# Optimization experiments

Hardware: AMD Instinct MI355X
Metric: run time of the kernel (lower is better)

The kernel has to match this reference:

```python
import jax, jax.numpy as jnp
import numpy as np

# Norse-style LIF constants (LIFParameters defaults, method='super', alpha=100)
DT = 0.001
TAU_SYN_INV = 200.0
TAU_MEM_INV = 100.0
V_TH = 1.0
V_LEAK = 0.0
V_RESET = 0.0
ALPHA = 100.0

@jax.custom_vjp
def heaviside(x):
    return (x > 0).astype(x.dtype)

def _heaviside_fwd(x):
    return heaviside(x), x

def _heaviside_bwd(x, g):
    # SuperSpike surrogate: 1 / (alpha*|x| + 1)^2
    return (g / (ALPHA * jnp.abs(x) + 1.0) ** 2,)

heaviside.defvjp(_heaviside_fwd, _heaviside_bwd)

def lif_step(v, i, inp_cur):
    # explicit-Euler LIF: membrane decays toward leak driven by synaptic current,
    # synaptic current decays, spikes reset membrane, input arrives as current jump
    v_dec = v + DT * TAU_MEM_INV * ((V_LEAK - v) + i)
    i_dec = i * (1.0 - DT * TAU_SYN_INV)
    z = heaviside(v_dec - V_TH)
    v_new = (1.0 - z) * v_dec + z * V_RESET
    i_new = i_dec + inp_cur
    return z, v_new, i_new

def li_step(v, i, inp_cur):
    # leaky integrator (non-spiking readout)
    v_new = v + DT * TAU_MEM_INV * ((V_LEAK - v) + i)
    i_new = i * (1.0 - DT * TAU_SYN_INV) + inp_cur
    return v_new, i_new


def setup_inputs() -> dict:
    key = jax.random.key(0)
    k1, k2, k3 = jax.random.split(key, 3)
    T, B = 64, 128
    FS2, H1, HC, OC, OUT = 4096, 2048, 2, 4, 10
    spl1, spl2 = FS2 // HC, H1 // OC
    x = jax.random.uniform(k1, (T, B, FS2), dtype=jnp.float32)
    w_hidden = jax.random.normal(k2, (HC, spl1, H1), dtype=jnp.float32) / np.sqrt(spl1)
    w_out = jax.random.normal(k3, (OC, spl2, OUT), dtype=jnp.float32) / np.sqrt(spl2)
    return {"x": x, "w_hidden": w_hidden, "w_out": w_out}


def reference(x, w_hidden, w_out):
    T, B, FS2 = x.shape
    HC, SPL1, H1 = w_hidden.shape
    OC, SPL2, OUT = w_out.shape
    f32 = x.dtype

    def step(carry, x_t):
        vdh, idh, vsh, ish, vdo, ido, vso, iso = carry
        # split input across hidden dendritic channels: [HC, B, SPL1]
        zc = x_t.reshape(B, HC, SPL1).transpose(1, 0, 2)
        cur_h = jnp.einsum('cbi,cio->cbo', zc, w_hidden)      # [HC, B, H1]
        s_d, vdh, idh = lif_step(vdh, idh, cur_h)             # dendritic spikes
        z_s, vsh, ish = lif_step(vsh, ish, s_d.sum(0))        # somatic spikes [B, H1]
        # split hidden spikes across output dendritic channels: [OC, B, SPL2]
        zo = z_s.reshape(B, OC, SPL2).transpose(1, 0, 2)
        cur_o = jnp.einsum('cbi,cio->cbo', zo, w_out)         # [OC, B, OUT]
        s_o, vdo, ido = lif_step(vdo, ido, cur_o)
        vso, iso = li_step(vso, iso, s_o.sum(0))              # readout voltage [B, OUT]
        return (vdh, idh, vsh, ish, vdo, ido, vso, iso), vso

    z = jnp.zeros
    carry0 = (z((HC, B, H1), f32), z((HC, B, H1), f32),
              z((B, H1), f32), z((B, H1), f32),
              z((OC, B, OUT), f32), z((OC, B, OUT), f32),
              z((B, OUT), f32), z((B, OUT), f32))
    _, voltages = jax.lax.scan(step, carry0, x)
    return voltages  # [T, B, 10]
```

## Files before the change

kernel.cpp:

```cpp
#include <hip/hip_runtime.h>

#define B 128
#define HC 2
#define H1 2048
#define FS2 4096
#define NK 2048
#define OC 4
#define SPL2 512
#define NOUT 10
#define T 64
#define HBH (HC*B*H1)

typedef __attribute__((ext_vector_type(8))) short bf16x8;
typedef __attribute__((ext_vector_type(4))) float f32x4;

__device__ __forceinline__ unsigned short f2bf(float f) {
  unsigned u = __float_as_uint(f);
  u += 0x7fff + ((u >> 16) & 1);
  return (unsigned short)(u >> 16);
}
__device__ __forceinline__ float bf2f(unsigned short s) {
  return __uint_as_float(((unsigned)s) << 16);
}

__device__ __forceinline__ void gload16(const void* g, void* l) {
  __builtin_amdgcn_global_load_lds(
      (const __attribute__((address_space(1))) unsigned int*)g,
      (__attribute__((address_space(3))) unsigned int*)l, 16, 0, 0);
}

__global__ __launch_bounds__(256) void init_state(float* __restrict__ p, int n) {
  int i = blockIdx.x * 256 + threadIdx.x;
  if (i < n) p[i] = 0.f;
}

__global__ __launch_bounds__(256) void conv_x(
    const float4* __restrict__ xin, ushort4* __restrict__ xh,
    ushort4* __restrict__ xl, int n4) {
  for (int i = blockIdx.x * 256 + threadIdx.x; i < n4; i += gridDim.x * 256) {
    float4 v = xin[i];
    ushort4 h, lo;
    h.x = f2bf(v.x); h.y = f2bf(v.y); h.z = f2bf(v.z); h.w = f2bf(v.w);
    lo.x = f2bf(v.x - bf2f(h.x)); lo.y = f2bf(v.y - bf2f(h.y));
    lo.z = f2bf(v.z - bf2f(h.z)); lo.w = f2bf(v.w - bf2f(h.w));
    xh[i] = h; xl[i] = lo;
  }
}

__global__ __launch_bounds__(256) void conv_w(
    const float* __restrict__ w, unsigned short* __restrict__ wth,
    unsigned short* __restrict__ wtl) {
  __shared__ float s[64][65];
  const int c = blockIdx.z;
  const int n0 = blockIdx.x * 64, k0 = blockIdx.y * 64;
  const int tid = threadIdx.x;
  const int r = tid >> 4, c4 = (tid & 15) * 4;
#pragma unroll
  for (int q = 0; q < 4; ++q) {
    int kr = r + q * 16;
    float4 v = *(const float4*)(w + ((size_t)c * NK + k0 + kr) * H1 + n0 + c4);
    s[kr][c4 + 0] = v.x; s[kr][c4 + 1] = v.y;
    s[kr][c4 + 2] = v.z; s[kr][c4 + 3] = v.w;
  }
  __syncthreads();
#pragma unroll
  for (int q = 0; q < 4; ++q) {
    int nr = r + q * 16;
    float a0 = s[c4 + 0][nr], a1 = s[c4 + 1][nr];
    float a2 = s[c4 + 2][nr], a3 = s[c4 + 3][nr];
    ushort4 h, lo;
    h.x = f2bf(a0); h.y = f2bf(a1); h.z = f2bf(a2); h.w = f2bf(a3);
    lo.x = f2bf(a0 - bf2f(h.x)); lo.y = f2bf(a1 - bf2f(h.y));
    lo.z = f2bf(a2 - bf2f(h.z)); lo.w = f2bf(a3 - bf2f(h.w));
    size_t off = ((size_t)c * H1 + n0 + nr) * NK + k0 + c4;
    *(ushort4*)(wth + off) = h;
    *(ushort4*)(wtl + off) = lo;
  }
}

__global__ __launch_bounds__(512, 2) void gemm_split(
    const unsigned short* __restrict__ xh, const unsigned short* __restrict__ xl,
    const unsigned short* __restrict__ wth, const unsigned short* __restrict__ wtl,
    float* __restrict__ cur, int Mc, int nMblk) {
  const int bid = blockIdx.x;
  int c, nb, mb;
  if ((nMblk & 3) == 0) {
    const int xcd = bid & 7;
    const int slot = bid >> 3;
    c = xcd & 1;
    const int q = xcd >> 1;
    const int mq = nMblk >> 2;
    nb = slot & 7;
    mb = q * mq + (slot >> 3);
  } else {
    mb = bid % nMblk;
    int rest = bid / nMblk;
    nb = rest & 7;
    c = rest >> 3;
  }
  const int bm = mb * 256, bn = nb * 256;

  __shared__ unsigned short lds[65536];
  const int tid = threadIdx.x;

  unsigned dstOff[2]; size_t srcA[2], srcB[2];
#pragma unroll
  for (int q = 0; q < 2; ++q) {
    int idx = q * 512 + tid;
    int row = idx >> 2, ps = idx & 3;
    int ks = (ps - (row >> 1)) & 3;
    int ar = bm + row; if (ar > Mc - 1) ar = Mc - 1;
    srcA[q] = (size_t)ar * FS2 + (size_t)c * NK + ks * 8;
    srcB[q] = (size_t)c * NK * H1 + (size_t)(bn + row) * NK + ks * 8;
    dstOff[q] = idx * 8;
  }

  const int l = tid & 63, w = tid >> 6;
  const int wr = w >> 2, wc = w & 3;
  const int lrow = l & 15, lks = l >> 4;
  unsigned aoff[8], boff[4];
#pragma unroll
  for (int m = 0; m < 8; ++m) {
    int row = wr * 128 + m * 16 + lrow;
    int ps = (lks + (row >> 1)) & 3;
    aoff[m] = row * 32 + ps * 8;
  }
#pragma unroll
  for (int n = 0; n < 4; ++n) {
    int rn = wc * 64 + n * 16 + lrow;
    int ps = (lks + (rn >> 1)) & 3;
    boff[n] = rn * 32 + ps * 8;
  }

  f32x4 acc[8][4];
#pragma unroll
  for (int m = 0; m < 8; ++m)
#pragma unroll
    for (int n = 0; n < 4; ++n) acc[m][n] = (f32x4){0.f, 0.f, 0.f, 0.f};

#pragma unroll
  for (int q = 0; q < 2; ++q) {
    gload16(xh + srcA[q], &lds[dstOff[q]]);
    gload16(xl + srcA[q], &lds[8192 + dstOff[q]]);
    gload16(wth + srcB[q], &lds[16384 + dstOff[q]]);
    gload16(wtl + srcB[q], &lds[24576 + dstOff[q]]);
  }
  __syncthreads();

  const int NT = NK / 32;
  int curb = 0;
  for (int kt = 0; kt < NT; ++kt) {
    if (kt + 1 < NT) {
      const int k0 = (kt + 1) * 32;
      const unsigned nb0 = (curb ^ 1) * 32768;
#pragma unroll
      for (int q = 0; q < 2; ++q) {
        gload16(xh + srcA[q] + k0, &lds[nb0 + dstOff[q]]);
        gload16(xl + srcA[q] + k0, &lds[nb0 + 8192 + dstOff[q]]);
        gload16(wth + srcB[q] + k0, &lds[nb0 + 16384 + dstOff[q]]);
        gload16(wtl + srcB[q] + k0, &lds[nb0 + 24576 + dstOff[q]]);
      }
    }
    const unsigned short* bc = &lds[curb * 32768];
    bf16x8 bh[4], bl[4];
#pragma unroll
    for (int n = 0; n < 4; ++n) {
      bh[n] = *(const bf16x8*)&bc[16384 + boff[n]];
      bl[n] = *(const bf16x8*)&bc[24576 + boff[n]];
    }
#pragma unroll
    for (int mh = 0; mh < 2; ++mh) {
      bf16x8 ah[4], al[4];
#pragma unroll
      for (int mm = 0; mm < 4; ++mm) {
        ah[mm] = *(const bf16x8*)&bc[aoff[mh * 4 + mm]];
        al[mm] = *(const bf16x8*)&bc[8192 + aoff[mh * 4 + mm]];
      }
#pragma unroll
      for (int mm = 0; mm < 4; ++mm)
#pragma unroll
        for (int n = 0; n < 4; ++n) {
          int m = mh * 4 + mm;
          acc[m][n] = __builtin_amdgcn_mfma_f32_16x16x32_bf16(ah[mm], bh[n], acc[m][n], 0, 0, 0);
          acc[m][n] = __builtin_amdgcn_mfma_f32_16x16x32_bf16(ah[mm], bl[n], acc[m][n], 0, 0, 0);
          acc[m][n] = __builtin_amdgcn_mfma_f32_16x16x32_bf16(al[mm], bh[n], acc[m][n], 0, 0, 0);
        }
    }
    __syncthreads();
    curb ^= 1;
  }

  float* Cc = cur + (size_t)c * Mc * H1;
#pragma unroll
  for (int m = 0; m < 8; ++m) {
    int grow = bm + wr * 128 + m * 16 + (l >> 4) * 4;
    if (grow < Mc) {
#pragma unroll
      for (int n = 0; n < 4; ++n) {
        int gcol = bn + wc * 64 + n * 16 + (l & 15);
        float* Cp = Cc + (size_t)grow * H1 + gcol;
        Cp[0]      = acc[m][n][0];
        Cp[H1]     = acc[m][n][1];
        Cp[2 * H1] = acc[m][n][2];
        Cp[3 * H1] = acc[m][n][3];
      }
    }
  }
}

__global__ __launch_bounds__(256) void seq_chunk(
    const float* __restrict__ cur, const float* __restrict__ wout,
    float* __restrict__ vdh, float* __restrict__ idh,
    float* __restrict__ vsh, float* __restrict__ ish,
    float* __restrict__ vdo, float* __restrict__ ido,
    float* __restrict__ sp_g, int t0, int tc, int Mc) {
  const int b = blockIdx.x >> 2;
  const int oc = blockIdx.x & 3;
  const int tid = threadIdx.x;
  __shared__ float wols[SPL2 * NOUT];
  __shared__ float zls[SPL2];
  __shared__ float cols[16];

#pragma unroll
  for (int q = 0; q < 5; ++q) {
    int i4 = q * 256 + tid;
    ((float4*)wols)[i4] = ((const float4*)(wout + (size_t)oc * SPL2 * NOUT))[i4];
  }
  const int hb = oc * SPL2;
  float vdl[HC][2], idl[HC][2], vsl[2], isl[2];
#pragma unroll
  for (int c = 0; c < HC; ++c)
#pragma unroll
    for (int u = 0; u < 2; ++u) {
      size_t o = ((size_t)c * B + b) * H1 + hb + tid + u * 256;
      vdl[c][u] = vdh[o]; idl[c][u] = idh[o];
    }
#pragma unroll
  for (int u = 0; u < 2; ++u) {
    size_t o = (size_t)b * H1 + hb + tid + u * 256;
    vsl[u] = vsh[o]; isl[u] = ish[o];
  }
  float vo = 0.f, io = 0.f;
  if (tid < NOUT) {
    vo = vdo[(oc * B + b) * NOUT + tid];
    io = ido[(oc * B + b) * NOUT + tid];
  }
  float pc[HC][2];
#pragma unroll
  for (int c = 0; c < HC; ++c)
#pragma unroll
    for (int u = 0; u < 2; ++u)
      pc[c][u] = cur[((size_t)c * Mc + b) * H1 + hb + tid + u * 256];

  for (int tl = 0; tl < tc; ++tl) {
#pragma unroll
    for (int u = 0; u < 2; ++u) {
      float zsum = 0.f;
#pragma unroll
      for (int c = 0; c < HC; ++c) {
        float v = vdl[c][u], i = idl[c][u];
        float vdec = v + 0.1f * (i - v);
        float idec = 0.8f * i;
        bool z = (vdec - 1.0f) > 0.f;
        vdl[c][u] = z ? 0.f : vdec;
        idl[c][u] = idec + pc[c][u];
        zsum += z ? 1.f : 0.f;
      }
      float v = vsl[u], i = isl[u];
      float vdec = v + 0.1f * (i - v);
      float idec = 0.8f * i;
      bool z = (vdec - 1.0f) > 0.f;
      vsl[u] = z ? 0.f : vdec;
      isl[u] = idec + zsum;
      zls[tid + u * 256] = z ? 1.f : 0.f;
    }
    if (tl + 1 < tc) {
#pragma unroll
      for (int c = 0; c < HC; ++c)
#pragma unroll
        for (int u = 0; u < 2; ++u)
          pc[c][u] = cur[((size_t)c * Mc + (tl + 1) * B + b) * H1 + hb + tid + u * 256];
    }
    __syncthreads();
    {
      const int g = tid >> 4, li = tid & 15;
      if (g < NOUT) {
        float s = 0.f;
#pragma unroll
        for (int j = 0; j < 32; ++j) {
          int i2 = li + 16 * j;
          s += zls[i2] * wols[i2 * NOUT + g];
        }
        s += __shfl_xor(s, 1); s += __shfl_xor(s, 2);
        s += __shfl_xor(s, 4); s += __shfl_xor(s, 8);
        if (li == 0) cols[g] = s;
      }
    }
    __syncthreads();
    if (tid < NOUT) {
      float vdec = vo + 0.1f * (io - vo);
      float idec = 0.8f * io;
      bool z = (vdec - 1.0f) > 0.f;
      vo = z ? 0.f : vdec;
      io = idec + cols[tid];
      sp_g[((size_t)(t0 + tl) * B + b) * (OC * NOUT) + oc * NOUT + tid] = z ? 1.f : 0.f;
    }
  }

#pragma unroll
  for (int c = 0; c < HC; ++c)
#pragma unroll
    for (int u = 0; u < 2; ++u) {
      size_t o = ((size_t)c * B + b) * H1 + hb + tid + u * 256;
      vdh[o] = vdl[c][u]; idh[o] = idl[c][u];
    }
#pragma unroll
  for (int u = 0; u < 2; ++u) {
    size_t o = (size_t)b * H1 + hb + tid + u * 256;
    vsh[o] = vsl[u]; ish[o] = isl[u];
  }
  if (tid < NOUT) {
    vdo[(oc * B + b) * NOUT + tid] = vo;
    ido[(oc * B + b) * NOUT + tid] = io;
  }
}

__global__ __launch_bounds__(256) void integrate_out(
    const float* __restrict__ sp_g, float* __restrict__ out) {
  int i = blockIdx.x * 256 + threadIdx.x;
  if (i >= B * NOUT) return;
  int b = i / NOUT, o = i % NOUT;
  float vr = 0.f, ir = 0.f;
  for (int t = 0; t < T; ++t) {
    const float* p = sp_g + ((size_t)(t * B + b) * OC) * NOUT + o;
    float ssum = ((p[0] + p[NOUT]) + p[2 * NOUT]) + p[3 * NOUT];
    float vn = vr + 0.1f * (ir - vr);
    ir = 0.8f * ir + ssum;
    vr = vn;
    out[(size_t)(t * B + b) * NOUT + o] = vn;
  }
}

extern "C" void kernel_launch(void* const* d_in, const int* in_sizes, int n_in,
                              void* d_out, int out_size, void* d_ws, size_t ws_size,
                              hipStream_t stream) {
  const float* x  = (const float*)d_in[0];
  const float* wh = (const float*)d_in[1];
  const float* wo = (const float*)d_in[2];
  float* out = (float*)d_out;
  char* ws = (char*)d_ws;

  unsigned short* wth = (unsigned short*)ws;
  unsigned short* wtl = wth + (size_t)HC * NK * H1;
  float* st  = (float*)(wtl + (size_t)HC * NK * H1);
  float* vdh = st;
  float* idh = vdh + HBH;
  float* vsh = idh + HBH;
  float* ish = vsh + (size_t)B * H1;
  float* vdo = ish + (size_t)B * H1;
  float* ido = vdo + OC * B * NOUT;
  float* sp_g = ido + OC * B * NOUT;
  float* dyn = sp_g + (size_t)T * B * OC * NOUT;
  const int NSTATE = (int)(sp_g - st);

  size_t fixed_bytes = (size_t)((char*)dyn - ws);
  size_t avail = (ws_size > fixed_bytes + 256) ? ws_size - fixed_bytes - 256 : 0;
  const size_t per_t = (size_t)HC * B * H1 * 4 + (size_t)B * FS2 * 2 * 2;
  int Tc = (int)(avail / per_t);
  if (Tc > T) Tc = T;
  if (Tc >= 2) Tc &= ~1;
  if (Tc < 1) Tc = 1;

  float* cur = dyn;
  unsigned short* xh = (unsigned short*)(cur + (size_t)Tc * HC * B * H1);
  unsigned short* xl = xh + (size_t)Tc * B * FS2;

  init_state<<<(NSTATE + 255) / 256, 256, 0, stream>>>(st, NSTATE);
  conv_w<<<dim3(H1 / 64, NK / 64, HC), 256, 0, stream>>>(wh, wth, wtl);

  for (int t0 = 0; t0 < T; t0 += Tc) {
    int tc = (T - t0 < Tc) ? (T - t0) : Tc;
    int Mc = tc * B;
    int n4 = Mc * (FS2 / 4);
    int cb = (n4 + 255) / 256; if (cb > 2048) cb = 2048;
    conv_x<<<cb, 256, 0, stream>>>((const float4*)(x + (size_t)t0 * B * FS2),
                                   (ushort4*)xh, (ushort4*)xl, n4);
    int nMblk = (Mc + 255) / 256;
    gemm_split<<<HC * 8 * nMblk, 512, 0, stream>>>(xh, xl, wth, wtl, cur, Mc, nMblk);
    seq_chunk<<<B * OC, 256, 0, stream>>>(cur, wo, vdh, idh, vsh, ish,
                                          vdo, ido, sp_g, t0, tc, Mc);
  }
  integrate_out<<<(B * NOUT + 255) / 256, 256, 0, stream>>>(sp_g, out);
}
```

Baseline: 441.7 us.

## Split GEMM K-step into three phased stages with fine-grained vmcnt waits

Restructures the double-buffered split-bf16 GEMM main loop into three phases (hi*hi, hi*lo, lo*hi). Each phase issues the next tile's loads for one operand, then waits only on the matching outstanding loads with explicit s_waitcnt vmcnt plus s_barrier instead of a full __syncthreads. The aim is to overlap global-to-LDS transfers with MFMA work more finely, and s_setprio raises wave priority around the MFMA blocks. In exchange it relies on hand-counted vmcnt values and on the asm barriers ordering LDS reuse correctly, which is fragile.

```diff
diff --git a/kernel.cpp b/kernel.cpp
--- a/kernel.cpp
+++ b/kernel.cpp
@@ -138,56 +138,99 @@
 #pragma unroll
     for (int n = 0; n < 4; ++n) acc[m][n] = (f32x4){0.f, 0.f, 0.f, 0.f};
 
-#pragma unroll
-  for (int q = 0; q < 2; ++q) {
-    gload16(xh + srcA[q], &lds[dstOff[q]]);
-    gload16(xl + srcA[q], &lds[8192 + dstOff[q]]);
-    gload16(wth + srcB[q], &lds[16384 + dstOff[q]]);
-    gload16(wtl + srcB[q], &lds[24576 + dstOff[q]]);
-  }
-  __syncthreads();
+  gload16(xh  + srcA[0], &lds[dstOff[0]]);
+  gload16(xh  + srcA[1], &lds[dstOff[1]]);
+  gload16(wth + srcB[0], &lds[16384 + dstOff[0]]);
+  gload16(wth + srcB[1], &lds[16384 + dstOff[1]]);
+  gload16(wtl + srcB[0], &lds[24576 + dstOff[0]]);
+  gload16(wtl + srcB[1], &lds[24576 + dstOff[1]]);
+  gload16(xl  + srcA[0], &lds[8192 + dstOff[0]]);
+  gload16(xl  + srcA[1], &lds[8192 + dstOff[1]]);
 
   const int NT = NK / 32;
-  int curb = 0;
-  for (int kt = 0; kt < NT; ++kt) {
-    if (kt + 1 < NT) {
-      const int k0 = (kt + 1) * 32;
-      const unsigned nb0 = (curb ^ 1) * 32768;
-#pragma unroll
-      for (int q = 0; q < 2; ++q) {
-        gload16(xh + srcA[q] + k0, &lds[nb0 + dstOff[q]]);
-        gload16(xl + srcA[q] + k0, &lds[nb0 + 8192 + dstOff[q]]);
-        gload16(wth + srcB[q] + k0, &lds[nb0 + 16384 + dstOff[q]]);
-        gload16(wtl + srcB[q] + k0, &lds[nb0 + 24576 + dstOff[q]]);
-      }
-    }
-    const unsigned short* bc = &lds[curb * 32768];
-    bf16x8 bh[4], bl[4];
-#pragma unroll
-    for (int n = 0; n < 4; ++n) {
-      bh[n] = *(const bf16x8*)&bc[16384 + boff[n]];
-      bl[n] = *(const bf16x8*)&bc[24576 + boff[n]];
-    }
-#pragma unroll
-    for (int mh = 0; mh < 2; ++mh) {
-      bf16x8 ah[4], al[4];
-#pragma unroll
-      for (int mm = 0; mm < 4; ++mm) {
-        ah[mm] = *(const bf16x8*)&bc[aoff[mh * 4 + mm]];
-        al[mm] = *(const bf16x8*)&bc[8192 + aoff[mh * 4 + mm]];
-      }
-#pragma unroll
-      for (int mm = 0; mm < 4; ++mm)
-#pragma unroll
-        for (int n = 0; n < 4; ++n) {
-          int m = mh * 4 + mm;
-          acc[m][n] = __builtin_amdgcn_mfma_f32_16x16x32_bf16(ah[mm], bh[n], acc[m][n], 0, 0, 0);
-          acc[m][n] = __builtin_amdgcn_mfma_f32_16x16x32_bf16(ah[mm], bl[n], acc[m][n], 0, 0, 0);
-          acc[m][n] = __builtin_amdgcn_mfma_f32_16x16x32_bf16(al[mm], bh[n], acc[m][n], 0, 0, 0);
-        }
-    }
-    __syncthreads();
-    curb ^= 1;
+  for (int t = 0; t < NT - 1; ++t) {
+    const unsigned cb   = (unsigned)(t & 1) * 32768;
+    const unsigned nbuf = (unsigned)((t + 1) & 1) * 32768;
+    const int kn = (t + 1) * 32;
+
+    asm volatile("s_waitcnt vmcnt(4)\ns_barrier" ::: "memory");
+    gload16(xh  + srcA[0] + kn, &lds[nbuf + dstOff[0]]);
+    gload16(xh  + srcA[1] + kn, &lds[nbuf + dstOff[1]]);
+    gload16(wth + srcB[0] + kn, &lds[nbuf + 16384 + dstOff[0]]);
+    gload16(wth + srcB[1] + kn, &lds[nbuf + 16384 + dstOff[1]]);
+    bf16x8 bh[4], ah[8];
+#pragma unroll
+    for (int n = 0; n < 4; ++n) bh[n] = *(const bf16x8*)&lds[cb + 16384 + boff[n]];
+#pragma unroll
+    for (int m = 0; m < 8; ++m) ah[m] = *(const bf16x8*)&lds[cb + aoff[m]];
+    __builtin_amdgcn_s_setprio(1);
+#pragma unroll
+    for (int m = 0; m < 8; ++m)
+#pragma unroll
+      for (int n = 0; n < 4; ++n)
+        acc[m][n] = __builtin_amdgcn_mfma_f32_16x16x32_bf16(ah[m], bh[n], acc[m][n], 0, 0, 0);
+    __builtin_amdgcn_s_setprio(0);
+
+    asm volatile("s_waitcnt vmcnt(6)\ns_barrier" ::: "memory");
+    gload16(wtl + srcB[0] + kn, &lds[nbuf + 24576 + dstOff[0]]);
+    gload16(wtl + srcB[1] + kn, &lds[nbuf + 24576 + dstOff[1]]);
+    bf16x8 bl[4];
+#pragma unroll
+    for (int n = 0; n < 4; ++n) bl[n] = *(const bf16x8*)&lds[cb + 24576 + boff[n]];
+    __builtin_amdgcn_s_setprio(1);
+#pragma unroll
+    for (int m = 0; m < 8; ++m)
+#pragma unroll
+      for (int n = 0; n < 4; ++n)
+        acc[m][n] = __builtin_amdgcn_mfma_f32_16x16x32_bf16(ah[m], bl[n], acc[m][n], 0, 0, 0);
+    __builtin_amdgcn_s_setprio(0);
+
+    asm volatile("s_waitcnt vmcnt(6)\ns_barrier" ::: "memory");
+    gload16(xl + srcA[0] + kn, &lds[nbuf + 8192 + dstOff[0]]);
+    gload16(xl + srcA[1] + kn, &lds[nbuf + 8192 + dstOff[1]]);
+    bf16x8 al[8];
+#pragma unroll
+    for (int m = 0; m < 8; ++m) al[m] = *(const bf16x8*)&lds[cb + 8192 + aoff[m]];
+    __builtin_amdgcn_s_setprio(1);
+#pragma unroll
+    for (int m = 0; m < 8; ++m)
+#pragma unroll
+      for (int n = 0; n < 4; ++n)
+        acc[m][n] = __builtin_amdgcn_mfma_f32_16x16x32_bf16(al[m], bh[n], acc[m][n], 0, 0, 0);
+    __builtin_amdgcn_s_setprio(0);
+  }
+
+  {
+    const unsigned cb = (unsigned)((NT - 1) & 1) * 32768;
+    asm volatile("s_waitcnt vmcnt(4)\ns_barrier" ::: "memory");
+    bf16x8 bh[4], ah[8];
+#pragma unroll
+    for (int n = 0; n < 4; ++n) bh[n] = *(const bf16x8*)&lds[cb + 16384 + boff[n]];
+#pragma unroll
+    for (int m = 0; m < 8; ++m) ah[m] = *(const bf16x8*)&lds[cb + aoff[m]];
+#pragma unroll
+    for (int m = 0; m < 8; ++m)
+#pragma unroll
+      for (int n = 0; n < 4; ++n)
+        acc[m][n] = __builtin_amdgcn_mfma_f32_16x16x32_bf16(ah[m], bh[n], acc[m][n], 0, 0, 0);
+    asm volatile("s_waitcnt vmcnt(2)\ns_barrier" ::: "memory");
+    bf16x8 bl[4];
+#pragma unroll
+    for (int n = 0; n < 4; ++n) bl[n] = *(const bf16x8*)&lds[cb + 24576 + boff[n]];
+#pragma unroll
+    for (int m = 0; m < 8; ++m)
+#pragma unroll
+      for (int n = 0; n < 4; ++n)
+        acc[m][n] = __builtin_amdgcn_mfma_f32_16x16x32_bf16(ah[m], bl[n], acc[m][n], 0, 0, 0);
+    asm volatile("s_waitcnt vmcnt(0)\ns_barrier" ::: "memory");
+    bf16x8 al[8];
+#pragma unroll
+    for (int m = 0; m < 8; ++m) al[m] = *(const bf16x8*)&lds[cb + 8192 + aoff[m]];
+#pragma unroll
+    for (int m = 0; m < 8; ++m)
+#pragma unroll
+      for (int n = 0; n < 4; ++n)
+        acc[m][n] = __builtin_amdgcn_mfma_f32_16x16x32_bf16(al[m], bh[n], acc[m][n], 0, 0, 0);
   }
 
   float* Cc = cur + (size_t)c * Mc * H1;
```

After: 427.5 us (median of 2 runs). 3.2% less time.
